# Performance work log

Measured on AMD Instinct MI355X. Metric: run time of the kernel, lower is better.

## Reference

```python
import jax, jax.numpy as jnp
import numpy as np

B, S, L, H, C = 16, 2048, 256, 768, 512

def setup_inputs() -> dict:
    key = jax.random.key(0)
    ks = jax.random.split(key, 9)
    sc = 1.0 / np.sqrt(H)
    return {
        "input_hidden_states": jax.random.normal(ks[0], (B, S, H), jnp.float32),
        "label_hidden_states": jax.random.normal(ks[1], (L, H), jnp.float32),
        "Wi": jax.random.normal(ks[2], (C, H), jnp.float32) * sc,
        "bi": jnp.zeros((C,), jnp.float32),
        "Wl": jax.random.normal(ks[3], (C, H), jnp.float32) * sc,
        "bl": jnp.zeros((C,), jnp.float32),
        "Wia": jax.random.normal(ks[4], (C, H), jnp.float32) * sc,
        "bia": jnp.zeros((C,), jnp.float32),
        "Wla": jax.random.normal(ks[5], (C, H), jnp.float32) * sc,
        "bla": jnp.zeros((C,), jnp.float32),
        "context": jax.random.uniform(ks[6], (C,), jnp.float32),
        "Wp": jax.random.normal(ks[7], (H, C), jnp.float32) * (1.0 / np.sqrt(C)),
    }

def reference(input_hidden_states, label_hidden_states, Wi, bi, Wl, bl,
              Wia, bia, Wla, bla, context, Wp):
    # Dropout is identity in eval mode.
    x = input_hidden_states            # [B,S,H]
    lab = label_hidden_states          # [L,H] (original repeats over batch; math is identical)
    input_trans = jax.nn.sigmoid(jnp.einsum('bsh,ch->bsc', x, Wi) + bi)      # [B,S,C]
    label_trans = jax.nn.sigmoid(lab @ Wl.T + bl)                            # [L,C]
    input_attn = jax.nn.sigmoid(jnp.einsum('bsh,ch->bsc', x, Wia) + bia)    # [B,S,C]
    label_attn = jax.nn.sigmoid(lab @ Wla.T + bla)                          # [L,C]
    # attn logits: (context * input_attn) @ label_attn^T  -> [B,S,L]
    logits = jnp.einsum('bsc,lc->bsl', input_attn * context, label_attn)
    attn = jax.nn.softmax(logits, axis=-1)                                   # [B,S,L]
    # trilinear reduction: sum_{s,l} input_trans[b,s,c] * attn[b,s,l] * label_trans[l,c]
    weighted = jnp.einsum('bsl,lc->bsc', attn, label_trans)                  # [B,S,C]
    fusion = jnp.sum(input_trans * weighted, axis=1)                         # [B,C]
    return fusion @ Wp.T                                                     # [B,H]
```

## Files before the change

kernel.cpp:

```cpp
#include <hip/hip_runtime.h>

#define H_DIM 768
#define C_DIM 512
#define L_DIM 256
#define S_DIM 2048
#define B_DIM 16

#define IA_STRIDE 520
#define ATTN_STRIDE 264
#define XP_STRIDE 776

typedef __attribute__((ext_vector_type(8))) short short8;
typedef __attribute__((ext_vector_type(4))) float f32x4;
typedef __attribute__((ext_vector_type(2))) __fp16 half2v;

#define MFMA_F16(a, b, c) __builtin_amdgcn_mfma_f32_16x16x32_f16((a), (b), (c), 0, 0, 0)

__device__ __forceinline__ unsigned short f2h(float f) {
    _Float16 h = (_Float16)f;
    return __builtin_bit_cast(unsigned short, h);
}
__device__ __forceinline__ float h2f(unsigned short u) {
    _Float16 h = __builtin_bit_cast(_Float16, u);
    return (float)h;
}
__device__ __forceinline__ float sigmoid_f(float x) { return 1.0f / (1.0f + __expf(-x)); }

__device__ __forceinline__ short8 cvt8(const float* p) {
    const float4* q = (const float4*)(const void*)p;
    float4 u = q[0], v = q[1];
    half2v h0 = __builtin_amdgcn_cvt_pkrtz(u.x, u.y);
    half2v h1 = __builtin_amdgcn_cvt_pkrtz(u.z, u.w);
    half2v h2 = __builtin_amdgcn_cvt_pkrtz(v.x, v.y);
    half2v h3 = __builtin_amdgcn_cvt_pkrtz(v.z, v.w);
    int4 pk = { __builtin_bit_cast(int, h0), __builtin_bit_cast(int, h1),
                __builtin_bit_cast(int, h2), __builtin_bit_cast(int, h3) };
    return __builtin_bit_cast(short8, pk);
}


__global__ __launch_bounds__(256) void prep_all(
    const float* __restrict__ x,
    const float* __restrict__ Wi, const float* __restrict__ Wia,
    const float* __restrict__ lab,
    const float* __restrict__ Wl,  const float* __restrict__ bl,
    const float* __restrict__ Wla, const float* __restrict__ bla,
    const float* __restrict__ ctx,
    unsigned short* __restrict__ x_f,
    unsigned short* __restrict__ Wi_f, unsigned short* __restrict__ Wia_f,
    unsigned short* __restrict__ la_f, unsigned short* __restrict__ lt_f,
    float* __restrict__ fusion)
{
    __shared__ unsigned short tile[16 * XP_STRIDE];
    const int t   = threadIdx.x;
    const int bid = blockIdx.x;

    if (bid == 0) {
        float4 z = {0.f, 0.f, 0.f, 0.f};
        float4* fp = (float4*)(void*)fusion;
#pragma unroll
        for (int i = 0; i < 8; ++i) fp[i * 256 + t] = z;
        return;
    }

    if (bid < 65) {
        const int lbid = bid - 1;
        const int wave = t >> 6;
        const int lane = t & 63;
        const int quad = lane >> 4;
        const int c16  = lane & 15;
        const int ct2  = lbid & 7;
        const int mh   = lbid >> 3;
        const int ct   = ct2 * 4 + wave;
        const int n0   = ct * 16;
        const int l0   = mh * 32;

        const f32x4 z4 = {0.f, 0.f, 0.f, 0.f};
        f32x4 a1[2], a2[2];
#pragma unroll
        for (int mt = 0; mt < 2; ++mt) { a1[mt] = z4; a2[mt] = z4; }

        const float* lb   = lab + (size_t)(l0 + c16) * H_DIM + quad * 8;
        const float* wlp  = Wl  + (size_t)(n0 + c16) * H_DIM + quad * 8;
        const float* wlap = Wla + (size_t)(n0 + c16) * H_DIM + quad * 8;
        for (int kt = 0; kt < 24; ++kt) {
            short8 b1 = cvt8(wlp + kt * 32);
            short8 b2 = cvt8(wlap + kt * 32);
#pragma unroll
            for (int mt = 0; mt < 2; ++mt) {
                short8 a = cvt8(lb + mt * 16 * H_DIM + kt * 32);
                a1[mt] = MFMA_F16(a, b1, a1[mt]);
                a2[mt] = MFMA_F16(a, b2, a2[mt]);
            }
        }
        const int c = n0 + c16;
        const float blv = bl[c], blav = bla[c], cv = ctx[c];
#pragma unroll
        for (int mt = 0; mt < 2; ++mt)
#pragma unroll
            for (int r = 0; r < 4; ++r) {
                const int l = l0 + mt * 16 + quad * 4 + r;
                const float ltv = sigmoid_f(a1[mt][r] + blv);
                const float lav = sigmoid_f(a2[mt][r] + blav) * cv;
                {
                    const int ctc = c >> 4, ktl = l >> 5;
                    const int frag = ((ctc >> 3) * 8 + ktl) * 8 + (ctc & 7);
                    const int ln = (c & 15) | (((l >> 3) & 3) << 4);
                    lt_f[((size_t)frag * 64 + ln) * 8 + (l & 7)] = f2h(ltv);
                }
                {
                    const int lt = l >> 4, ktc = c >> 5;
                    const int frag = ((lt >> 2) * 16 + ktc) * 4 + (lt & 3);
                    const int ln = (l & 15) | (((c >> 3) & 3) << 4);
                    la_f[((size_t)frag * 64 + ln) * 8 + (c & 7)] = f2h(lav);
                }
            }
        return;
    }

    if (bid < 449) {
        const int tid = (bid - 65) * 256 + t;
        const int m   = tid / 49152;
        const int idx = tid - m * 49152;
        const int ct   = idx / 1536;
        const int rem  = idx - ct * 1536;
        const int kt   = rem >> 6;
        const int lane = rem & 63;
        const int row  = ct * 16 + (lane & 15);
        const int kcol = kt * 32 + (lane >> 4) * 8;
        const float* src = (m == 0 ? Wi : Wia);
        unsigned short* dst = (m == 0 ? Wi_f : Wia_f);
        short8 v = cvt8(src + (size_t)row * H_DIM + kcol);
        const int frag = ((ct >> 3) * 24 + kt) * 8 + (ct & 7);
        *(short8*)(void*)(dst + ((size_t)frag * 64 + lane) * 8) = v;
        return;
    }

    {
        const int mt = bid - 449;
        const float4* src = (const float4*)(const void*)(x + (size_t)mt * 16 * H_DIM);
#pragma unroll
        for (int i = 0; i < 12; ++i) {
            const int id  = i * 256 + t;
            const int row = id / 192;
            const int c4  = id - row * 192;
            float4 v = src[id];
            half2v h0 = __builtin_amdgcn_cvt_pkrtz(v.x, v.y);
            half2v h1 = __builtin_amdgcn_cvt_pkrtz(v.z, v.w);
            uint2 pk = { __builtin_bit_cast(unsigned int, h0),
                         __builtin_bit_cast(unsigned int, h1) };
            *(uint2*)(void*)(tile + row * XP_STRIDE + c4 * 4) = pk;
        }
        __syncthreads();
        const int lane = t & 63;
        const int wave = t >> 6;
#pragma unroll
        for (int q = 0; q < 6; ++q) {
            const int kt = wave * 6 + q;
            short8 v = *(const short8*)(const void*)(
                tile + (lane & 15) * XP_STRIDE + kt * 32 + (lane >> 4) * 8);
            *(short8*)(void*)(x_f + ((size_t)(mt * 24 + kt) * 64 + lane) * 8) = v;
        }
    }
}

template<bool XF>
__global__ __launch_bounds__(512, 4) void fused_main(
    const unsigned short* __restrict__ x_f,
    const float* __restrict__ x,
    const float* __restrict__ bi,
    const float* __restrict__ bia,
    const unsigned short* __restrict__ Wi_f,
    const unsigned short* __restrict__ Wia_f,
    const unsigned short* __restrict__ lt_f,
    const unsigned short* __restrict__ la_f,
    float* __restrict__ fusion)
{
    __shared__ unsigned short lds_buf[64 * IA_STRIDE];
    __shared__ float scratchA[8 * 64];
    __shared__ float scratchB[8 * 64];
    __shared__ float inv_lds[64];

    const int tid  = threadIdx.x;
    const int wave = tid >> 6;
    const int lane = tid & 63;
    const int quad = lane >> 4;
    const int c16  = lane & 15;

    const int row0 = blockIdx.x * 64;
    const int b    = row0 >> 11;

    const f32x4 z4 = {0.f, 0.f, 0.f, 0.f};
    const int n0 = wave * 64;

    const float*  xb  = x + (size_t)(row0 + c16) * H_DIM + quad * 8;
    const short8* xf8 = (const short8*)(const void*)x_f + (size_t)blockIdx.x * 96 * 64 + lane;
    const size_t wofs = ((size_t)(wave >> 1) * 192 + (size_t)(wave & 1) * 4) * 64 + lane;

    {
        f32x4 acc[4][4];
#pragma unroll
        for (int m = 0; m < 4; ++m)
#pragma unroll
            for (int nt = 0; nt < 4; ++nt) acc[m][nt] = z4;
        const short8* wa8 = (const short8*)(const void*)Wia_f + wofs;
        for (int kt = 0; kt < 24; ++kt) {
            short8 a0, a1, a2, a3;
            if constexpr (XF) {
                a0 = xf8[kt * 64];        a1 = xf8[(24 + kt) * 64];
                a2 = xf8[(48 + kt) * 64]; a3 = xf8[(72 + kt) * 64];
            } else {
                a0 = cvt8(xb + kt * 32);                a1 = cvt8(xb + 16 * H_DIM + kt * 32);
                a2 = cvt8(xb + 32 * H_DIM + kt * 32);   a3 = cvt8(xb + 48 * H_DIM + kt * 32);
            }
#pragma unroll
            for (int nt = 0; nt < 4; ++nt) {
                short8 bw = wa8[(kt * 8 + nt) * 64];
                acc[0][nt] = MFMA_F16(a0, bw, acc[0][nt]);
                acc[1][nt] = MFMA_F16(a1, bw, acc[1][nt]);
                acc[2][nt] = MFMA_F16(a2, bw, acc[2][nt]);
                acc[3][nt] = MFMA_F16(a3, bw, acc[3][nt]);
            }
        }
#pragma unroll
        for (int nt = 0; nt < 4; ++nt) {
            const int col = n0 + nt * 16 + c16;
            const float bv = bia[col];
#pragma unroll
            for (int m = 0; m < 4; ++m)
#pragma unroll
                for (int r = 0; r < 4; ++r) {
                    const int row = m * 16 + quad * 4 + r;
                    lds_buf[row * IA_STRIDE + col] = f2h(sigmoid_f(acc[m][nt][r] + bv));
                }
        }
    }
    __syncthreads();

    const int n0l = wave * 32;
    f32x4 accl[4][2];
#pragma unroll
    for (int m = 0; m < 4; ++m)
#pragma unroll
        for (int j = 0; j < 2; ++j) accl[m][j] = z4;
    {
        const unsigned short* ab = lds_buf + c16 * IA_STRIDE + quad * 8;
        const short8* la8 = (const short8*)(const void*)la_f
                          + ((size_t)(wave >> 1) * 64 + (size_t)(wave & 1) * 2) * 64 + lane;
        for (int kt = 0; kt < 16; ++kt) {
            const int kk = kt * 32;
            short8 a0 = *(const short8*)(const void*)(ab + kk);
            short8 a1 = *(const short8*)(const void*)(ab + 16 * IA_STRIDE + kk);
            short8 a2 = *(const short8*)(const void*)(ab + 32 * IA_STRIDE + kk);
            short8 a3 = *(const short8*)(const void*)(ab + 48 * IA_STRIDE + kk);
#pragma unroll
            for (int j = 0; j < 2; ++j) {
                short8 bfr = la8[(kt * 4 + j) * 64];
                accl[0][j] = MFMA_F16(a0, bfr, accl[0][j]);
                accl[1][j] = MFMA_F16(a1, bfr, accl[1][j]);
                accl[2][j] = MFMA_F16(a2, bfr, accl[2][j]);
                accl[3][j] = MFMA_F16(a3, bfr, accl[3][j]);
            }
        }
    }
    __syncthreads();

#pragma unroll
    for (int m = 0; m < 4; ++m)
#pragma unroll
        for (int r = 0; r < 4; ++r) {
            float mx = fmaxf(accl[m][0][r], accl[m][1][r]);
#pragma unroll
            for (int off = 1; off < 16; off <<= 1) mx = fmaxf(mx, __shfl_xor(mx, off, 64));
            if (c16 == 0) scratchA[wave * 64 + m * 16 + quad * 4 + r] = mx;
        }
    __syncthreads();
#pragma unroll
    for (int m = 0; m < 4; ++m)
#pragma unroll
        for (int r = 0; r < 4; ++r) {
            const int row = m * 16 + quad * 4 + r;
            float gm = scratchA[row];
#pragma unroll
            for (int w = 1; w < 8; ++w) gm = fmaxf(gm, scratchA[w * 64 + row]);
            const float e0 = __expf(accl[m][0][r] - gm);
            const float e1 = __expf(accl[m][1][r] - gm);
            lds_buf[row * ATTN_STRIDE + n0l + c16]      = f2h(e0);
            lds_buf[row * ATTN_STRIDE + n0l + 16 + c16] = f2h(e1);
            float s = e0 + e1;
#pragma unroll
            for (int off = 1; off < 16; off <<= 1) s += __shfl_xor(s, off, 64);
            if (c16 == 0) scratchB[wave * 64 + row] = s;
        }
    __syncthreads();
    if (wave == 0 && c16 == 0) {
#pragma unroll
        for (int m = 0; m < 4; ++m)
#pragma unroll
            for (int r = 0; r < 4; ++r) {
                const int row = m * 16 + quad * 4 + r;
                float st = 0.f;
#pragma unroll
                for (int w = 0; w < 8; ++w) st += scratchB[w * 64 + row];
                inv_lds[row] = 1.0f / st;
            }
    }

    f32x4 accw[4][4];
#pragma unroll
    for (int m = 0; m < 4; ++m)
#pragma unroll
        for (int nt = 0; nt < 4; ++nt) accw[m][nt] = z4;
    {
        const unsigned short* ab = lds_buf + c16 * ATTN_STRIDE + quad * 8;
        const short8* lt8 = (const short8*)(const void*)lt_f
                          + ((size_t)(wave >> 1) * 64 + (size_t)(wave & 1) * 4) * 64 + lane;
        for (int kt = 0; kt < 8; ++kt) {
            const int kk = kt * 32;
            short8 a0 = *(const short8*)(const void*)(ab + kk);
            short8 a1 = *(const short8*)(const void*)(ab + 16 * ATTN_STRIDE + kk);
            short8 a2 = *(const short8*)(const void*)(ab + 32 * ATTN_STRIDE + kk);
            short8 a3 = *(const short8*)(const void*)(ab + 48 * ATTN_STRIDE + kk);
#pragma unroll
            for (int nt = 0; nt < 4; ++nt) {
                short8 bfr = lt8[(kt * 8 + nt) * 64];
                accw[0][nt] = MFMA_F16(a0, bfr, accw[0][nt]);
                accw[1][nt] = MFMA_F16(a1, bfr, accw[1][nt]);
                accw[2][nt] = MFMA_F16(a2, bfr, accw[2][nt]);
                accw[3][nt] = MFMA_F16(a3, bfr, accw[3][nt]);
            }
        }
    }
    __syncthreads();

    {
        float invr[4][4];
#pragma unroll
        for (int m = 0; m < 4; ++m)
#pragma unroll
            for (int r = 0; r < 4; ++r) invr[m][r] = inv_lds[m * 16 + quad * 4 + r];
#pragma unroll
        for (int nt = 0; nt < 4; ++nt) {
            const int col = n0 + nt * 16 + c16;
#pragma unroll
            for (int m = 0; m < 4; ++m)
#pragma unroll
                for (int r = 0; r < 4; ++r) {
                    const int row = m * 16 + quad * 4 + r;
                    lds_buf[row * IA_STRIDE + col] = f2h(accw[m][nt][r] * invr[m][r]);
                }
        }
    }

    {
        f32x4 acc[4][4];
#pragma unroll
        for (int m = 0; m < 4; ++m)
#pragma unroll
            for (int nt = 0; nt < 4; ++nt) acc[m][nt] = z4;
        const short8* wi8 = (const short8*)(const void*)Wi_f + wofs;
        for (int kt = 0; kt < 24; ++kt) {
            short8 a0, a1, a2, a3;
            if constexpr (XF) {
                a0 = xf8[kt * 64];        a1 = xf8[(24 + kt) * 64];
                a2 = xf8[(48 + kt) * 64]; a3 = xf8[(72 + kt) * 64];
            } else {
                a0 = cvt8(xb + kt * 32);                a1 = cvt8(xb + 16 * H_DIM + kt * 32);
                a2 = cvt8(xb + 32 * H_DIM + kt * 32);   a3 = cvt8(xb + 48 * H_DIM + kt * 32);
            }
#pragma unroll
            for (int nt = 0; nt < 4; ++nt) {
                short8 bw = wi8[(kt * 8 + nt) * 64];
                acc[0][nt] = MFMA_F16(a0, bw, acc[0][nt]);
                acc[1][nt] = MFMA_F16(a1, bw, acc[1][nt]);
                acc[2][nt] = MFMA_F16(a2, bw, acc[2][nt]);
                acc[3][nt] = MFMA_F16(a3, bw, acc[3][nt]);
            }
        }
#pragma unroll
        for (int nt = 0; nt < 4; ++nt) {
            const int col = n0 + nt * 16 + c16;
            const float bv = bi[col];
            float s = 0.f;
#pragma unroll
            for (int m = 0; m < 4; ++m)
#pragma unroll
                for (int r = 0; r < 4; ++r) {
                    const int row = m * 16 + quad * 4 + r;
                    s += h2f(lds_buf[row * IA_STRIDE + col]) * sigmoid_f(acc[m][nt][r] + bv);
                }
            s += __shfl_xor(s, 16, 64);
            s += __shfl_xor(s, 32, 64);
            if (lane < 16) atomicAdd(&fusion[b * C_DIM + col], s);
        }
    }
}

__global__ __launch_bounds__(256) void out_kernel(
    const float* __restrict__ fusion,
    const float* __restrict__ Wp,
    float* __restrict__ out)
{
    const int idx = blockIdx.x * 256 + threadIdx.x;
    const int R   = idx >> 3;
    const int sub = idx & 7;
    const int bb  = R / H_DIM;
    const int h   = R - bb * H_DIM;
    const float* wp = Wp + (size_t)h * C_DIM;
    const float* f  = fusion + bb * C_DIM;
    float s = 0.f;
#pragma unroll
    for (int j = 0; j < 16; ++j) {
        const int c = j * 32 + sub * 4;
        float4 wv = *(const float4*)(const void*)(wp + c);
        float4 fv = *(const float4*)(const void*)(f + c);
        s += fv.x * wv.x + fv.y * wv.y + fv.z * wv.z + fv.w * wv.w;
    }
    s += __shfl_xor(s, 1, 64);
    s += __shfl_xor(s, 2, 64);
    s += __shfl_xor(s, 4, 64);
    if (sub == 0) out[R] = s;
}

extern "C" void kernel_launch(void* const* d_in, const int* in_sizes, int n_in,
                              void* d_out, int out_size, void* d_ws, size_t ws_size,
                              hipStream_t stream)
{
    const float* x    = (const float*)d_in[0];
    const float* lab  = (const float*)d_in[1];
    const float* Wi   = (const float*)d_in[2];
    const float* bi   = (const float*)d_in[3];
    const float* Wl   = (const float*)d_in[4];
    const float* bl   = (const float*)d_in[5];
    const float* Wia  = (const float*)d_in[6];
    const float* bia  = (const float*)d_in[7];
    const float* Wla  = (const float*)d_in[8];
    const float* bla  = (const float*)d_in[9];
    const float* ctx  = (const float*)d_in[10];
    const float* Wp   = (const float*)d_in[11];

    char* ws = (char*)d_ws;
    unsigned short* Wi_f  = (unsigned short*)(ws);
    unsigned short* Wia_f = (unsigned short*)(ws + 786432);
    unsigned short* la_f  = (unsigned short*)(ws + 3145728);
    unsigned short* lt_f  = (unsigned short*)(ws + 3407872);
    float* fusion         = (float*)(ws + 3670016);
    unsigned short* x_f   = (unsigned short*)(ws + 3702784);
    const size_t NEED_XF  = 3702784 + (size_t)32768 * 768 * 2;

    if (ws_size >= NEED_XF) {
        prep_all<<<2497, 256, 0, stream>>>(
            x, Wi, Wia, lab, Wl, bl, Wla, bla, ctx,
            x_f, Wi_f, Wia_f, la_f, lt_f, fusion);
        fused_main<true><<<(B_DIM * S_DIM) / 64, 512, 0, stream>>>(
            x_f, x, bi, bia, Wi_f, Wia_f, lt_f, la_f, fusion);
    } else {
        prep_all<<<449, 256, 0, stream>>>(
            x, Wi, Wia, lab, Wl, bl, Wla, bla, ctx,
            nullptr, Wi_f, Wia_f, la_f, lt_f, fusion);
        fused_main<false><<<(B_DIM * S_DIM) / 64, 512, 0, stream>>>(
            nullptr, x, bi, bia, Wi_f, Wia_f, lt_f, la_f, fusion);
    }
    out_kernel<<<384, 256, 0, stream>>>(fusion, Wp, (float*)d_out);
}
```

Before: 286.7 us.

## Merge prep, main and output kernels into one persistent kernel with grid barriers

Replaces the three-launch sequence (prep_all, fused_main, out_kernel) with one 512-block kernel. Inside it, software grid barriers built on atomic counters separate the weight/label preprocessing and fp16 conversion of x, the fused attention/trilinear stage, and the final projection. The fusion buffer and counters are zeroed by a memset instead of a dedicated block. This removes launch gaps and tail effects between stages, but it relies on all 512 blocks being co-resident (4 per CU) and adds spin-wait barrier overhead. The main stage keeps the fixed 64-rows-per-block mapping.

Result: slower. 541.9 us (+89.0%).

```diff
diff --git a/kernel.cpp b/kernel.cpp
--- a/kernel.cpp
+++ b/kernel.cpp
@@ -38,48 +38,55 @@
     return __builtin_bit_cast(short8, pk);
 }
 
-
-__global__ __launch_bounds__(256) void prep_all(
-    const float* __restrict__ x,
-    const float* __restrict__ Wi, const float* __restrict__ Wia,
-    const float* __restrict__ lab,
+__device__ __forceinline__ void grid_barrier(unsigned* cnt, unsigned target) {
+    __syncthreads();
+    if (threadIdx.x == 0) {
+        __threadfence();
+        atomicAdd(cnt, 1u);
+        while (__hip_atomic_load(cnt, __ATOMIC_ACQUIRE, __HIP_MEMORY_SCOPE_AGENT) < target) {
+            __builtin_amdgcn_s_sleep(8);
+        }
+    }
+    __syncthreads();
+}
+
+
+__global__ __launch_bounds__(512, 4) void mega(
+    const float* __restrict__ x,   const float* __restrict__ lab,
+    const float* __restrict__ Wi,  const float* __restrict__ bi,
     const float* __restrict__ Wl,  const float* __restrict__ bl,
+    const float* __restrict__ Wia, const float* __restrict__ bia,
     const float* __restrict__ Wla, const float* __restrict__ bla,
-    const float* __restrict__ ctx,
+    const float* __restrict__ ctx, const float* __restrict__ Wp,
     unsigned short* __restrict__ x_f,
     unsigned short* __restrict__ Wi_f, unsigned short* __restrict__ Wia_f,
     unsigned short* __restrict__ la_f, unsigned short* __restrict__ lt_f,
-    float* __restrict__ fusion)
+    float* __restrict__ fusion, unsigned* __restrict__ cnt,
+    float* __restrict__ out)
 {
-    __shared__ unsigned short tile[16 * XP_STRIDE];
-    const int t   = threadIdx.x;
-    const int bid = blockIdx.x;
-
-    if (bid == 0) {
-        float4 z = {0.f, 0.f, 0.f, 0.f};
-        float4* fp = (float4*)(void*)fusion;
-#pragma unroll
-        for (int i = 0; i < 8; ++i) fp[i * 256 + t] = z;
-        return;
-    }
-
-    if (bid < 65) {
-        const int lbid = bid - 1;
-        const int wave = t >> 6;
-        const int lane = t & 63;
-        const int quad = lane >> 4;
-        const int c16  = lane & 15;
-        const int ct2  = lbid & 7;
-        const int mh   = lbid >> 3;
-        const int ct   = ct2 * 4 + wave;
-        const int n0   = ct * 16;
-        const int l0   = mh * 32;
-
-        const f32x4 z4 = {0.f, 0.f, 0.f, 0.f};
+    __shared__ unsigned short lds_buf[64 * IA_STRIDE];
+    __shared__ float scratchA[8 * 64];
+    __shared__ float scratchB[8 * 64];
+    __shared__ float inv_lds[64];
+
+    const int tid  = threadIdx.x;
+    const int wave = tid >> 6;
+    const int lane = tid & 63;
+    const int quad = lane >> 4;
+    const int c16  = lane & 15;
+    const int bid  = blockIdx.x;
+
+    const f32x4 z4 = {0.f, 0.f, 0.f, 0.f};
+
+    if (bid < 32) {
+        const int s  = bid * 8 + wave;
+        const int ct = s & 31;
+        const int mh = s >> 5;
+        const int n0 = ct * 16;
+        const int l0 = mh * 32;
         f32x4 a1[2], a2[2];
 #pragma unroll
         for (int mt = 0; mt < 2; ++mt) { a1[mt] = z4; a2[mt] = z4; }
-
         const float* lb   = lab + (size_t)(l0 + c16) * H_DIM + quad * 8;
         const float* wlp  = Wl  + (size_t)(n0 + c16) * H_DIM + quad * 8;
         const float* wlap = Wla + (size_t)(n0 + c16) * H_DIM + quad * 8;
@@ -115,61 +122,361 @@
                     la_f[((size_t)frag * 64 + ln) * 8 + (c & 7)] = f2h(lav);
                 }
             }
-        return;
-    }
-
-    if (bid < 449) {
-        const int tid = (bid - 65) * 256 + t;
-        const int m   = tid / 49152;
-        const int idx = tid - m * 49152;
+    }
+
+    {
+        unsigned short* tile = lds_buf;
+#pragma unroll 1
+        for (int tt = 0; tt < 4; ++tt) {
+            const int mt = bid * 4 + tt;
+            const float4* src = (const float4*)(const void*)(x + (size_t)mt * 16 * H_DIM);
+            __syncthreads();
+#pragma unroll
+            for (int i = 0; i < 6; ++i) {
+                const int id  = i * 512 + tid;
+                const int row = id / 192;
+                const int c4  = id - row * 192;
+                float4 v = src[id];
+                half2v h0 = __builtin_amdgcn_cvt_pkrtz(v.x, v.y);
+                half2v h1 = __builtin_amdgcn_cvt_pkrtz(v.z, v.w);
+                uint2 pk = { __builtin_bit_cast(unsigned int, h0),
+                             __builtin_bit_cast(unsigned int, h1) };
+                *(uint2*)(void*)(tile + row * XP_STRIDE + c4 * 4) = pk;
+            }
+            __syncthreads();
+#pragma unroll
+            for (int q = 0; q < 3; ++q) {
+                const int kt = wave * 3 + q;
+                short8 v = *(const short8*)(const void*)(
+                    tile + (lane & 15) * XP_STRIDE + kt * 32 + (lane >> 4) * 8);
+                *(short8*)(void*)(x_f + ((size_t)(mt * 24 + kt) * 64 + lane) * 8) = v;
+            }
+        }
+    }
+
+    if (tid < 192) {
+        const int unit = bid * 192 + tid;
+        const int m    = unit / 49152;
+        const int idx  = unit - m * 49152;
         const int ct   = idx / 1536;
         const int rem  = idx - ct * 1536;
         const int kt   = rem >> 6;
-        const int lane = rem & 63;
-        const int row  = ct * 16 + (lane & 15);
-        const int kcol = kt * 32 + (lane >> 4) * 8;
+        const int ln   = rem & 63;
+        const int row  = ct * 16 + (ln & 15);
+        const int kcol = kt * 32 + (ln >> 4) * 8;
         const float* src = (m == 0 ? Wi : Wia);
         unsigned short* dst = (m == 0 ? Wi_f : Wia_f);
         short8 v = cvt8(src + (size_t)row * H_DIM + kcol);
         const int frag = ((ct >> 3) * 24 + kt) * 8 + (ct & 7);
-        *(short8*)(void*)(dst + ((size_t)frag * 64 + lane) * 8) = v;
+        *(short8*)(void*)(dst + ((size_t)frag * 64 + ln) * 8) = v;
+    }
+
+    grid_barrier(&cnt[0], gridDim.x);
+
+    const int row0 = bid * 64;
+    const int b    = row0 >> 11;
+    const int n0   = wave * 64;
+
+    const short8* xf8 = (const short8*)(const void*)x_f + (size_t)bid * 96 * 64 + lane;
+    const size_t wofs = ((size_t)(wave >> 1) * 192 + (size_t)(wave & 1) * 4) * 64 + lane;
+
+    {
+        f32x4 acc[4][4];
+#pragma unroll
+        for (int m = 0; m < 4; ++m)
+#pragma unroll
+            for (int nt = 0; nt < 4; ++nt) acc[m][nt] = z4;
+        const short8* wa8 = (const short8*)(const void*)Wia_f + wofs;
+        for (int kt = 0; kt < 24; ++kt) {
+            short8 a0 = xf8[kt * 64];
+            short8 a1 = xf8[(24 + kt) * 64];
+            short8 a2 = xf8[(48 + kt) * 64];
+            short8 a3 = xf8[(72 + kt) * 64];
+#pragma unroll
+            for (int nt = 0; nt < 4; ++nt) {
+                short8 bw = wa8[(kt * 8 + nt) * 64];
+                acc[0][nt] = MFMA_F16(a0, bw, acc[0][nt]);
+                acc[1][nt] = MFMA_F16(a1, bw, acc[1][nt]);
+                acc[2][nt] = MFMA_F16(a2, bw, acc[2][nt]);
+                acc[3][nt] = MFMA_F16(a3, bw, acc[3][nt]);
+            }
+        }
+#pragma unroll
+        for (int nt = 0; nt < 4; ++nt) {
+            const int col = n0 + nt * 16 + c16;
+            const float bv = bia[col];
+#pragma unroll
+            for (int m = 0; m < 4; ++m)
+#pragma unroll
+                for (int r = 0; r < 4; ++r) {
+                    const int row = m * 16 + quad * 4 + r;
+                    lds_buf[row * IA_STRIDE + col] = f2h(sigmoid_f(acc[m][nt][r] + bv));
+                }
+        }
+    }
+    __syncthreads();
+
+    const int n0l = wave * 32;
+    f32x4 accl[4][2];
+#pragma unroll
+    for (int m = 0; m < 4; ++m)
+#pragma unroll
+        for (int j = 0; j < 2; ++j) accl[m][j] = z4;
+    {
+        const unsigned short* ab = lds_buf + c16 * IA_STRIDE + quad * 8;
+        const short8* la8 = (const short8*)(const void*)la_f
+                          + ((size_t)(wave >> 1) * 64 + (size_t)(wave & 1) * 2) * 64 + lane;
+        for (int kt = 0; kt < 16; ++kt) {
+            const int kk = kt * 32;
+            short8 a0 = *(const short8*)(const void*)(ab + kk);
+            short8 a1 = *(const short8*)(const void*)(ab + 16 * IA_STRIDE + kk);
+            short8 a2 = *(const short8*)(const void*)(ab + 32 * IA_STRIDE + kk);
+            short8 a3 = *(const short8*)(const void*)(ab + 48 * IA_STRIDE + kk);
+#pragma unroll
+            for (int j = 0; j < 2; ++j) {
+                short8 bfr = la8[(kt * 4 + j) * 64];
+                accl[0][j] = MFMA_F16(a0, bfr, accl[0][j]);
+                accl[1][j] = MFMA_F16(a1, bfr, accl[1][j]);
+                accl[2][j] = MFMA_F16(a2, bfr, accl[2][j]);
+                accl[3][j] = MFMA_F16(a3, bfr, accl[3][j]);
+            }
+        }
+    }
+    __syncthreads();
+
+#pragma unroll
+    for (int m = 0; m < 4; ++m)
+#pragma unroll
+        for (int r = 0; r < 4; ++r) {
+            float mx = fmaxf(accl[m][0][r], accl[m][1][r]);
+#pragma unroll
+            for (int off = 1; off < 16; off <<= 1) mx = fmaxf(mx, __shfl_xor(mx, off, 64));
+            if (c16 == 0) scratchA[wave * 64 + m * 16 + quad * 4 + r] = mx;
+        }
+    __syncthreads();
+#pragma unroll
+    for (int m = 0; m < 4; ++m)
+#pragma unroll
+        for (int r = 0; r < 4; ++r) {
+            const int row = m * 16 + quad * 4 + r;
+            float gm = scratchA[row];
+#pragma unroll
+            for (int w = 1; w < 8; ++w) gm = fmaxf(gm, scratchA[w * 64 + row]);
+            const float e0 = __expf(accl[m][0][r] - gm);
+            const float e1 = __expf(accl[m][1][r] - gm);
+            lds_buf[row * ATTN_STRIDE + n0l + c16]      = f2h(e0);
+            lds_buf[row * ATTN_STRIDE + n0l + 16 + c16] = f2h(e1);
+            float s = e0 + e1;
+#pragma unroll
+            for (int off = 1; off < 16; off <<= 1) s += __shfl_xor(s, off, 64);
+            if (c16 == 0) scratchB[wave * 64 + row] = s;
+        }
+    __syncthreads();
+    if (wave == 0 && c16 == 0) {
+#pragma unroll
+        for (int m = 0; m < 4; ++m)
+#pragma unroll
+            for (int r = 0; r < 4; ++r) {
+                const int row = m * 16 + quad * 4 + r;
+                float st = 0.f;
+#pragma unroll
+                for (int w = 0; w < 8; ++w) st += scratchB[w * 64 + row];
+                inv_lds[row] = 1.0f / st;
+            }
+    }
+
+    f32x4 accw[4][4];
+#pragma unroll
+    for (int m = 0; m < 4; ++m)
+#pragma unroll
+        for (int nt = 0; nt < 4; ++nt) accw[m][nt] = z4;
+    {
+        const unsigned short* ab = lds_buf + c16 * ATTN_STRIDE + quad * 8;
+        const short8* lt8 = (const short8*)(const void*)lt_f
+                          + ((size_t)(wave >> 1) * 64 + (size_t)(wave & 1) * 4) * 64 + lane;
+        for (int kt = 0; kt < 8; ++kt) {
+            const int kk = kt * 32;
+            short8 a0 = *(const short8*)(const void*)(ab + kk);
+            short8 a1 = *(const short8*)(const void*)(ab + 16 * ATTN_STRIDE + kk);
+            short8 a2 = *(const short8*)(const void*)(ab + 32 * ATTN_STRIDE + kk);
+            short8 a3 = *(const short8*)(const void*)(ab + 48 * ATTN_STRIDE + kk);
+#pragma unroll
+            for (int nt = 0; nt < 4; ++nt) {
+                short8 bfr = lt8[(kt * 8 + nt) * 64];
+                accw[0][nt] = MFMA_F16(a0, bfr, accw[0][nt]);
+                accw[1][nt] = MFMA_F16(a1, bfr, accw[1][nt]);
+                accw[2][nt] = MFMA_F16(a2, bfr, accw[2][nt]);
+                accw[3][nt] = MFMA_F16(a3, bfr, accw[3][nt]);
+            }
+        }
+    }
+    __syncthreads();
+
+    {
+        float invr[4][4];
+#pragma unroll
+        for (int m = 0; m < 4; ++m)
+#pragma unroll
+            for (int r = 0; r < 4; ++r) invr[m][r] = inv_lds[m * 16 + quad * 4 + r];
+#pragma unroll
+        for (int nt = 0; nt < 4; ++nt) {
+            const int col = n0 + nt * 16 + c16;
+#pragma unroll
+            for (int m = 0; m < 4; ++m)
+#pragma unroll
+                for (int r = 0; r < 4; ++r) {
+                    const int row = m * 16 + quad * 4 + r;
+                    lds_buf[row * IA_STRIDE + col] = f2h(accw[m][nt][r] * invr[m][r]);
+                }
+        }
+    }
+
+    {
+        f32x4 acc[4][4];
+#pragma unroll
+        for (int m = 0; m < 4; ++m)
+#pragma unroll
+            for (int nt = 0; nt < 4; ++nt) acc[m][nt] = z4;
+        const short8* wi8 = (const short8*)(const void*)Wi_f + wofs;
+        for (int kt = 0; kt < 24; ++kt) {
+            short8 a0 = xf8[kt * 64];
+            short8 a1 = xf8[(24 + kt) * 64];
+            short8 a2 = xf8[(48 + kt) * 64];
+            short8 a3 = xf8[(72 + kt) * 64];
+#pragma unroll
+            for (int nt = 0; nt < 4; ++nt) {
+                short8 bw = wi8[(kt * 8 + nt) * 64];
+                acc[0][nt] = MFMA_F16(a0, bw, acc[0][nt]);
+                acc[1][nt] = MFMA_F16(a1, bw, acc[1][nt]);
+                acc[2][nt] = MFMA_F16(a2, bw, acc[2][nt]);
+                acc[3][nt] = MFMA_F16(a3, bw, acc[3][nt]);
+            }
+        }
+#pragma unroll
+        for (int nt = 0; nt < 4; ++nt) {
+            const int col = n0 + nt * 16 + c16;
+            const float bv = bi[col];
+            float s = 0.f;
+#pragma unroll
+            for (int m = 0; m < 4; ++m)
+#pragma unroll
+                for (int r = 0; r < 4; ++r) {
+                    const int row = m * 16 + quad * 4 + r;
+                    s += h2f(lds_buf[row * IA_STRIDE + col]) * sigmoid_f(acc[m][nt][r] + bv);
+                }
+            s += __shfl_xor(s, 16, 64);
+            s += __shfl_xor(s, 32, 64);
+            if (lane < 16) atomicAdd(&fusion[b * C_DIM + col], s);
+        }
+    }
+
+    grid_barrier(&cnt[1], gridDim.x);
+
+    if (tid < 192) {
+        const int j   = tid >> 3;
+        const int sub = tid & 7;
+        const int R   = bid * 24 + j;
+        const int bb  = R / H_DIM;
+        const int h   = R - bb * H_DIM;
+        const float* wp = Wp + (size_t)h * C_DIM;
+        const float* f  = fusion + bb * C_DIM;
+        float s = 0.f;
+#pragma unroll
+        for (int k = 0; k < 16; ++k) {
+            const int c = k * 32 + sub * 4;
+            float4 wv = *(const float4*)(const void*)(wp + c);
+            const float f0 = __hip_atomic_load(f + c + 0, __ATOMIC_RELAXED, __HIP_MEMORY_SCOPE_AGENT);
+            const float f1 = __hip_atomic_load(f + c + 1, __ATOMIC_RELAXED, __HIP_MEMORY_SCOPE_AGENT);
+            const float f2 = __hip_atomic_load(f + c + 2, __ATOMIC_RELAXED, __HIP_MEMORY_SCOPE_AGENT);
+            const float f3 = __hip_atomic_load(f + c + 3, __ATOMIC_RELAXED, __HIP_MEMORY_SCOPE_AGENT);
+            s += f0 * wv.x + f1 * wv.y + f2 * wv.z + f3 * wv.w;
+        }
+        s += __shfl_xor(s, 1, 64);
+        s += __shfl_xor(s, 2, 64);
+        s += __shfl_xor(s, 4, 64);
+        if (sub == 0) out[R] = s;
+    }
+}
+
+__global__ __launch_bounds__(256) void prep_small(
+    const float* __restrict__ Wi, const float* __restrict__ Wia,
+    const float* __restrict__ lab,
+    const float* __restrict__ Wl,  const float* __restrict__ bl,
+    const float* __restrict__ Wla, const float* __restrict__ bla,
+    const float* __restrict__ ctx,
+    unsigned short* __restrict__ Wi_f, unsigned short* __restrict__ Wia_f,
+    unsigned short* __restrict__ la_f, unsigned short* __restrict__ lt_f)
+{
+    const int t   = threadIdx.x;
+    const int bid = blockIdx.x;
+    if (bid < 64) {
+        const int wave = t >> 6;
+        const int lane = t & 63;
+        const int quad = lane >> 4;
+        const int c16  = lane & 15;
+        const int ct   = (bid & 7) * 4 + wave;
+        const int n0   = ct * 16;
+        const int l0   = (bid >> 3) * 32;
+        const f32x4 z4 = {0.f, 0.f, 0.f, 0.f};
+        f32x4 a1[2], a2[2];
+#pragma unroll
+        for (int mt = 0; mt < 2; ++mt) { a1[mt] = z4; a2[mt] = z4; }
+        const float* lb   = lab + (size_t)(l0 + c16) * H_DIM + quad * 8;
+        const float* wlp  = Wl  + (size_t)(n0 + c16) * H_DIM + quad * 8;
+        const float* wlap = Wla + (size_t)(n0 + c16) * H_DIM + quad * 8;
+        for (int kt = 0; kt < 24; ++kt) {
+            short8 b1 = cvt8(wlp + kt * 32);
+            short8 b2 = cvt8(wlap + kt * 32);
+#pragma unroll
+            for (int mt = 0; mt < 2; ++mt) {
+                short8 a = cvt8(lb + mt * 16 * H_DIM + kt * 32);
+                a1[mt] = MFMA_F16(a, b1, a1[mt]);
+                a2[mt] = MFMA_F16(a, b2, a2[mt]);
+            }
+        }
+        const int c = n0 + c16;
+        const float blv = bl[c], blav = bla[c], cv = ctx[c];
+#pragma unroll
+        for (int mt = 0; mt < 2; ++mt)
+#pragma unroll
+            for (int r = 0; r < 4; ++r) {
+                const int l = l0 + mt * 16 + quad * 4 + r;
+                const float ltv = sigmoid_f(a1[mt][r] + blv);
+                const float lav = sigmoid_f(a2[mt][r] + blav) * cv;
+                {
+                    const int ctc = c >> 4, ktl = l >> 5;
+                    const int frag = ((ctc >> 3) * 8 + ktl) * 8 + (ctc & 7);
+                    const int ln = (c & 15) | (((l >> 3) & 3) << 4);
+                    lt_f[((size_t)frag * 64 + ln) * 8 + (l & 7)] = f2h(ltv);
+                }
+                {
+                    const int lt = l >> 4, ktc = c >> 5;
+                    const int frag = ((lt >> 2) * 16 + ktc) * 4 + (lt & 3);
+                    const int ln = (l & 15) | (((c >> 3) & 3) << 4);
+                    la_f[((size_t)frag * 64 + ln) * 8 + (c & 7)] = f2h(lav);
+                }
+            }
         return;
     }
-
-    {
-        const int mt = bid - 449;
-        const float4* src = (const float4*)(const void*)(x + (size_t)mt * 16 * H_DIM);
-#pragma unroll
-        for (int i = 0; i < 12; ++i) {
-            const int id  = i * 256 + t;
-            const int row = id / 192;
-            const int c4  = id - row * 192;
-            float4 v = src[id];
-            half2v h0 = __builtin_amdgcn_cvt_pkrtz(v.x, v.y);
-            half2v h1 = __builtin_amdgcn_cvt_pkrtz(v.z, v.w);
-            uint2 pk = { __builtin_bit_cast(unsigned int, h0),
-                         __builtin_bit_cast(unsigned int, h1) };
-            *(uint2*)(void*)(tile + row * XP_STRIDE + c4 * 4) = pk;
-        }
-        __syncthreads();
-        const int lane = t & 63;
-        const int wave = t >> 6;
-#pragma unroll
-        for (int q = 0; q < 6; ++q) {
-            const int kt = wave * 6 + q;
-            short8 v = *(const short8*)(const void*)(
-                tile + (lane & 15) * XP_STRIDE + kt * 32 + (lane >> 4) * 8);
-            *(short8*)(void*)(x_f + ((size_t)(mt * 24 + kt) * 64 + lane) * 8) = v;
-        }
-    }
-}
-
-template<bool XF>
-__global__ __launch_bounds__(512, 4) void fused_main(
-    const unsigned short* __restrict__ x_f,
+    const int tid2 = (bid - 64) * 256 + t;
+    const int m    = tid2 / 49152;
+    const int idx  = tid2 - m * 49152;
+    const int ct   = idx / 1536;
+    const int rem  = idx - ct * 1536;
+    const int kt   = rem >> 6;
+    const int lane = rem & 63;
+    const int row  = ct * 16 + (lane & 15);
+    const int kcol = kt * 32 + (lane >> 4) * 8;
+    const float* src = (m == 0 ? Wi : Wia);
+    unsigned short* dst = (m == 0 ? Wi_f : Wia_f);
+    short8 v = cvt8(src + (size_t)row * H_DIM + kcol);
+    const int frag = ((ct >> 3) * 24 + kt) * 8 + (ct & 7);
+    *(short8*)(void*)(dst + ((size_t)frag * 64 + lane) * 8) = v;
+}
+
+__global__ __launch_bounds__(512, 4) void fused_small(
     const float* __restrict__ x,
-    const float* __restrict__ bi,
-    const float* __restrict__ bia,
+    const float* __restrict__ bi,  const float* __restrict__ bia,
     const unsigned short* __restrict__ Wi_f,
     const unsigned short* __restrict__ Wia_f,
     const unsigned short* __restrict__ lt_f,
@@ -186,15 +493,11 @@
     const int lane = tid & 63;
     const int quad = lane >> 4;
     const int c16  = lane & 15;
-
     const int row0 = blockIdx.x * 64;
     const int b    = row0 >> 11;
-
     const f32x4 z4 = {0.f, 0.f, 0.f, 0.f};
     const int n0 = wave * 64;
-
-    const float*  xb  = x + (size_t)(row0 + c16) * H_DIM + quad * 8;
-    const short8* xf8 = (const short8*)(const void*)x_f + (size_t)blockIdx.x * 96 * 64 + lane;
+    const float* xb = x + (size_t)(row0 + c16) * H_DIM + quad * 8;
     const size_t wofs = ((size_t)(wave >> 1) * 192 + (size_t)(wave & 1) * 4) * 64 + lane;
 
     {
@@ -205,14 +508,10 @@
             for (int nt = 0; nt < 4; ++nt) acc[m][nt] = z4;
         const short8* wa8 = (const short8*)(const void*)Wia_f + wofs;
         for (int kt = 0; kt < 24; ++kt) {
-            short8 a0, a1, a2, a3;
-            if constexpr (XF) {
-                a0 = xf8[kt * 64];        a1 = xf8[(24 + kt) * 64];
-                a2 = xf8[(48 + kt) * 64]; a3 = xf8[(72 + kt) * 64];
-            } else {
-                a0 = cvt8(xb + kt * 32);                a1 = cvt8(xb + 16 * H_DIM + kt * 32);
-                a2 = cvt8(xb + 32 * H_DIM + kt * 32);   a3 = cvt8(xb + 48 * H_DIM + kt * 32);
-            }
+            short8 a0 = cvt8(xb + kt * 32);
+            short8 a1 = cvt8(xb + 16 * H_DIM + kt * 32);
+            short8 a2 = cvt8(xb + 32 * H_DIM + kt * 32);
+            short8 a3 = cvt8(xb + 48 * H_DIM + kt * 32);
 #pragma unroll
             for (int nt = 0; nt < 4; ++nt) {
                 short8 bw = wa8[(kt * 8 + nt) * 64];
@@ -229,14 +528,12 @@
 #pragma unroll
             for (int m = 0; m < 4; ++m)
 #pragma unroll
-                for (int r = 0; r < 4; ++r) {
-                    const int row = m * 16 + quad * 4 + r;
-                    lds_buf[row * IA_STRIDE + col] = f2h(sigmoid_f(acc[m][nt][r] + bv));
-                }
-        }
-    }
-    __syncthreads();
-
+                for (int r = 0; r < 4; ++r)
+                    lds_buf[(m * 16 + quad * 4 + r) * IA_STRIDE + col] =
+                        f2h(sigmoid_f(acc[m][nt][r] + bv));
+        }
+    }
+    __syncthreads();
     const int n0l = wave * 32;
     f32x4 accl[4][2];
 #pragma unroll
@@ -264,7 +561,6 @@
         }
     }
     __syncthreads();
-
 #pragma unroll
     for (int m = 0; m < 4; ++m)
 #pragma unroll
@@ -305,7 +601,6 @@
                 inv_lds[row] = 1.0f / st;
             }
     }
-
     f32x4 accw[4][4];
 #pragma unroll
     for (int m = 0; m < 4; ++m)
@@ -332,7 +627,6 @@
         }
     }
     __syncthreads();
-
     {
         float invr[4][4];
 #pragma unroll
@@ -345,13 +639,11 @@
 #pragma unroll
             for (int m = 0; m < 4; ++m)
 #pragma unroll
-                for (int r = 0; r < 4; ++r) {
-                    const int row = m * 16 + quad * 4 + r;
-                    lds_buf[row * IA_STRIDE + col] = f2h(accw[m][nt][r] * invr[m][r]);
-                }
-        }
-    }
-
+                for (int r = 0; r < 4; ++r)
+                    lds_buf[(m * 16 + quad * 4 + r) * IA_STRIDE + col] =
+                        f2h(accw[m][nt][r] * invr[m][r]);
+        }
+    }
     {
         f32x4 acc[4][4];
 #pragma unroll
@@ -360,14 +652,10 @@
             for (int nt = 0; nt < 4; ++nt) acc[m][nt] = z4;
         const short8* wi8 = (const short8*)(const void*)Wi_f + wofs;
         for (int kt = 0; kt < 24; ++kt) {
-            short8 a0, a1, a2, a3;
-            if constexpr (XF) {
-                a0 = xf8[kt * 64];        a1 = xf8[(24 + kt) * 64];
-                a2 = xf8[(48 + kt) * 64]; a3 = xf8[(72 + kt) * 64];
-            } else {
-                a0 = cvt8(xb + kt * 32);                a1 = cvt8(xb + 16 * H_DIM + kt * 32);
-                a2 = cvt8(xb + 32 * H_DIM + kt * 32);   a3 = cvt8(xb + 48 * H_DIM + kt * 32);
-            }
+            short8 a0 = cvt8(xb + kt * 32);
+            short8 a1 = cvt8(xb + 16 * H_DIM + kt * 32);
+            short8 a2 = cvt8(xb + 32 * H_DIM + kt * 32);
+            short8 a3 = cvt8(xb + 48 * H_DIM + kt * 32);
 #pragma unroll
             for (int nt = 0; nt < 4; ++nt) {
                 short8 bw = wi8[(kt * 8 + nt) * 64];
@@ -385,10 +673,9 @@
 #pragma unroll
             for (int m = 0; m < 4; ++m)
 #pragma unroll
-                for (int r = 0; r < 4; ++r) {
-                    const int row = m * 16 + quad * 4 + r;
-                    s += h2f(lds_buf[row * IA_STRIDE + col]) * sigmoid_f(acc[m][nt][r] + bv);
-                }
+                for (int r = 0; r < 4; ++r)
+                    s += h2f(lds_buf[(m * 16 + quad * 4 + r) * IA_STRIDE + col])
+                       * sigmoid_f(acc[m][nt][r] + bv);
             s += __shfl_xor(s, 16, 64);
             s += __shfl_xor(s, 32, 64);
             if (lane < 16) atomicAdd(&fusion[b * C_DIM + col], s);
@@ -442,24 +729,24 @@
     char* ws = (char*)d_ws;
     unsigned short* Wi_f  = (unsigned short*)(ws);
     unsigned short* Wia_f = (unsigned short*)(ws + 786432);
+    unsigned*       cnt   = (unsigned*)(ws + 1572864);
+    float*          fusion= (float*)(ws + 1573120);
     unsigned short* la_f  = (unsigned short*)(ws + 3145728);
     unsigned short* lt_f  = (unsigned short*)(ws + 3407872);
-    float* fusion         = (float*)(ws + 3670016);
     unsigned short* x_f   = (unsigned short*)(ws + 3702784);
     const size_t NEED_XF  = 3702784 + (size_t)32768 * 768 * 2;
 
+    (void)hipMemsetAsync(ws + 1572864, 0, 256 + B_DIM * C_DIM * sizeof(float), stream);
+
     if (ws_size >= NEED_XF) {
-        prep_all<<<2497, 256, 0, stream>>>(
-            x, Wi, Wia, lab, Wl, bl, Wla, bla, ctx,
-            x_f, Wi_f, Wia_f, la_f, lt_f, fusion);
-        fused_main<true><<<(B_DIM * S_DIM) / 64, 512, 0, stream>>>(
-            x_f, x, bi, bia, Wi_f, Wia_f, lt_f, la_f, fusion);
+        mega<<<512, 512, 0, stream>>>(
+            x, lab, Wi, bi, Wl, bl, Wia, bia, Wla, bla, ctx, Wp,
+            x_f, Wi_f, Wia_f, la_f, lt_f, fusion, cnt, (float*)d_out);
     } else {
-        prep_all<<<449, 256, 0, stream>>>(
-            x, Wi, Wia, lab, Wl, bl, Wla, bla, ctx,
-            nullptr, Wi_f, Wia_f, la_f, lt_f, fusion);
-        fused_main<false><<<(B_DIM * S_DIM) / 64, 512, 0, stream>>>(
-            nullptr, x, bi, bia, Wi_f, Wia_f, lt_f, la_f, fusion);
-    }
-    out_kernel<<<384, 256, 0, stream>>>(fusion, Wp, (float*)d_out);
-}
+        prep_small<<<448, 256, 0, stream>>>(
+            Wi, Wia, lab, Wl, bl, Wla, bla, ctx, Wi_f, Wia_f, la_f, lt_f);
+        fused_small<<<(B_DIM * S_DIM) / 64, 512, 0, stream>>>(
+            x, bi, bia, Wi_f, Wia_f, lt_f, la_f, fusion);
+        out_kernel<<<384, 256, 0, stream>>>(fusion, Wp, (float*)d_out);
+    }
+}
```
